# Optimization experiments

Hardware: AMD Instinct MI355X
Metric: run time of the kernel (lower is better)

## Reference

```python
import jax, jax.numpy as jnp
import numpy as np

B, T, V, C, L, H = 4, 1024, 32000, 768, 6, 12
HD = C // H  # head size 64
EPS = 1e-5


def _ln(x, s, b):
    mu = jnp.mean(x, axis=-1, keepdims=True)
    var = jnp.var(x, axis=-1, keepdims=True)
    return (x - mu) * jax.lax.rsqrt(var + EPS) * s + b


def setup_inputs() -> dict:
    key = jax.random.key(0)
    ks = jax.random.split(key, 12)
    p = lambda k, shape: jax.random.normal(k, shape, jnp.float32) * 0.02
    return {
        "idx": jax.random.randint(ks[0], (B, T), 0, V),
        "targets": jax.random.randint(ks[1], (B, T), 0, V),
        "tok_emb": p(ks[2], (V, C)),
        "pos_emb": p(ks[3], (T, C)),
        "Wq": p(ks[4], (L, H, C, HD)),
        "Wk": p(ks[5], (L, H, C, HD)),
        "Wv": p(ks[6], (L, H, C, HD)),
        "ln1_s": jnp.ones((L, C), jnp.float32),
        "ln1_b": jnp.zeros((L, C), jnp.float32),
        "ln2_s": jnp.ones((L, C), jnp.float32),
        "ln2_b": jnp.zeros((L, C), jnp.float32),
        "W1": p(ks[7], (L, C, 4 * C)),
        "b1": jnp.zeros((L, 4 * C), jnp.float32),
        "W2": p(ks[8], (L, 4 * C, C)),
        "b2": jnp.zeros((L, C), jnp.float32),
        "lnf_s": jnp.ones((C,), jnp.float32),
        "lnf_b": jnp.zeros((C,), jnp.float32),
        "Wout": p(ks[9], (C, V)),
        "bout": jnp.zeros((V,), jnp.float32),
    }


def reference(idx, targets, tok_emb, pos_emb, Wq, Wk, Wv, ln1_s, ln1_b, ln2_s, ln2_b,
              W1, b1, W2, b2, lnf_s, lnf_b, Wout, bout):
    x = tok_emb[idx] + pos_emb[None, :T, :]  # [B,T,C]
    mask = jnp.tril(jnp.ones((T, T), bool))
    scale = HD ** -0.5
    for l in range(L):  # fixed small layer count
        xn = _ln(x, ln1_s[l], ln1_b[l])
        q = jnp.einsum('btc,hcd->bhtd', xn, Wq[l])
        k = jnp.einsum('btc,hcd->bhtd', xn, Wk[l])
        v = jnp.einsum('btc,hcd->bhtd', xn, Wv[l])
        scores = jnp.einsum('bhtd,bhsd->bhts', q, k) * scale
        scores = jnp.where(mask[None, None], scores, -jnp.inf)
        w = jax.nn.softmax(scores, axis=-1)
        att = jnp.einsum('bhts,bhsd->bhtd', w, v)
        # concat heads in order, matching torch.cat over ModuleList
        x = x + att.transpose(0, 2, 1, 3).reshape(B, T, C)
        xn2 = _ln(x, ln2_s[l], ln2_b[l])
        h = jax.nn.relu(jnp.einsum('btc,cf->btf', xn2, W1[l]) + b1[l])
        x = x + jnp.einsum('btf,fc->btc', h, W2[l]) + b2[l]
    x = _ln(x, lnf_s, lnf_b)
    logits = jnp.einsum('btc,cv->btv', x, Wout) + bout
    logits = logits.reshape(B * T, V)
    lp = jax.nn.log_softmax(logits, axis=-1)
    loss = -jnp.mean(lp[jnp.arange(B * T), targets.reshape(-1)])
    return logits, loss
```

## Files before the change

kernel.cpp:

```cpp
#include <hip/hip_runtime.h>
#include <hip/hip_bf16.h>


typedef __attribute__((ext_vector_type(8))) short          bh8;
typedef __attribute__((ext_vector_type(4))) unsigned short us4;
typedef __attribute__((ext_vector_type(4))) float          fl4;

__device__ inline unsigned short f2b(float f) {
  unsigned u = __float_as_uint(f);
  return (unsigned short)((u + 0x7fffu + ((u >> 16) & 1u)) >> 16);
}

__global__ __launch_bounds__(256) void embed_kernel(
    const int* __restrict__ idx, const float* __restrict__ tok,
    const float* __restrict__ pos, float* __restrict__ x)
{
  int i = blockIdx.x * 256 + threadIdx.x;
  int bt = i / 768, c = i - bt * 768;
  int t = bt & 1023;
  x[i] = tok[(size_t)idx[bt] * 768 + c] + pos[t * 768 + c];
}

__global__ __launch_bounds__(256) void ln_bf16_kernel(
    const float* __restrict__ x, const float* __restrict__ s,
    const float* __restrict__ b, unsigned short* __restrict__ out)
{
  __shared__ float redS[4], redQ[4];
  int row = blockIdx.x, tid = threadIdx.x;
  const float* xr = x + (size_t)row * 768;
  float v0 = xr[tid], v1 = xr[tid + 256], v2 = xr[tid + 512];
  float sm = v0 + v1 + v2;
  float sq = v0 * v0 + v1 * v1 + v2 * v2;
#pragma unroll
  for (int m = 1; m < 64; m <<= 1) {
    sm += __shfl_xor(sm, m);
    sq += __shfl_xor(sq, m);
  }
  int wv = tid >> 6;
  if ((tid & 63) == 0) { redS[wv] = sm; redQ[wv] = sq; }
  __syncthreads();
  float ts = redS[0] + redS[1] + redS[2] + redS[3];
  float tq = redQ[0] + redQ[1] + redQ[2] + redQ[3];
  float mu = ts * (1.0f / 768.0f);
  float var = tq * (1.0f / 768.0f) - mu * mu;
  float inv = rsqrtf(var + 1e-5f);
  unsigned short* outr = out + (size_t)row * 768;
  outr[tid]       = f2b((v0 - mu) * inv * s[tid]       + b[tid]);
  outr[tid + 256] = f2b((v1 - mu) * inv * s[tid + 256] + b[tid + 256]);
  outr[tid + 512] = f2b((v2 - mu) * inv * s[tid + 512] + b[tid + 512]);
}

__global__ __launch_bounds__(256) void tconv_kernel(
    const float* __restrict__ src, unsigned short* __restrict__ dst,
    int K, int N)
{
  __shared__ float tt[64][65];
  int n0 = blockIdx.x * 64, k0 = blockIdx.y * 64;
  const float* s = src + (size_t)blockIdx.z * K * N;
  unsigned short* d = dst + (size_t)blockIdx.z * K * N;
  int tx = threadIdx.x & 63, g = threadIdx.x >> 6;
#pragma unroll
  for (int i = 0; i < 16; ++i) {
    int k = g * 16 + i;
    tt[k][tx] = s[(size_t)(k0 + k) * N + n0 + tx];
  }
  __syncthreads();
#pragma unroll
  for (int i = 0; i < 16; ++i) {
    int n = g * 16 + i;
    d[(size_t)(n0 + n) * K + k0 + tx] = f2b(tt[tx][n]);
  }
}

__global__ __launch_bounds__(256) void tqkv_kernel(
    const float* __restrict__ src, unsigned short* __restrict__ dst, int which)
{
  __shared__ float tt[64][65];
  int k0 = blockIdx.x * 64;
  int z = blockIdx.y;
  int l = z / 12, h = z - l * 12;
  const float* s = src + (size_t)z * 768 * 64;
  unsigned short* d = dst + (size_t)l * 2304 * 768 +
                      (size_t)(which * 768 + h * 64) * 768;
  int tx = threadIdx.x & 63, g = threadIdx.x >> 6;
#pragma unroll
  for (int i = 0; i < 16; ++i) {
    int k = g * 16 + i;
    tt[k][tx] = s[(size_t)(k0 + k) * 64 + tx];
  }
  __syncthreads();
#pragma unroll
  for (int i = 0; i < 16; ++i) {
    int n = g * 16 + i;
    d[(size_t)n * 768 + k0 + tx] = f2b(tt[tx][n]);
  }
}

template<int MODE>
__global__ __launch_bounds__(256) void gemm_bf16(
    const unsigned short* __restrict__ A, const unsigned short* __restrict__ Bt,
    const float* __restrict__ bias, float* __restrict__ OutF,
    unsigned short* __restrict__ OutH, int N, int K)
{
  __shared__ __align__(16) char As[128 * 64 * 2];
  __shared__ __align__(16) char Bs[128 * 64 * 2];
  const int tid = threadIdx.x;
  const int lane = tid & 63;
  const int wr = (tid >> 7) & 1, wc = (tid >> 6) & 1;
  const int m0 = blockIdx.y * 128, n0 = blockIdx.x * 128;
  const size_t Kb = (size_t)K * 2;

  fl4 acc[4][4] = {};
  const int o0 = tid * 16;
  const int rA = wr * 64 + (lane & 15);
  const int rB = wc * 64 + (lane & 15);
  const int kcol = (lane >> 4) << 4;
  const int sw = (lane & 7) << 4;

  auto ldAB = [&](int t, bh8* a, bh8* b) {
#pragma unroll
    for (int p = 0; p < 4; ++p) {
      int o = o0 + p * 4096;
      int row = o >> 7, col = o & 127;
      a[p] = *(const bh8*)((const char*)A + (size_t)(m0 + row) * Kb + (size_t)t * 128 + col);
      b[p] = *(const bh8*)((const char*)Bt + (size_t)(n0 + row) * Kb + (size_t)t * 128 + col);
    }
  };

  const int nK = K >> 6;
  bh8 ca[4], cb[4];
  ldAB(0, ca, cb);
  for (int t = 0; t < nK; ++t) {
    __syncthreads();
#pragma unroll
    for (int p = 0; p < 4; ++p) {
      int o = o0 + p * 4096;
      int row = o >> 7;
      int phys = o ^ ((row & 7) << 4);
      *(bh8*)(As + phys) = ca[p];
      *(bh8*)(Bs + phys) = cb[p];
    }
    __syncthreads();
    bh8 na[4], nb[4];
    const bool more = (t + 1 < nK);
    if (more) ldAB(t + 1, na, nb);
#pragma unroll
    for (int kh = 0; kh < 2; ++kh) {
      bh8 af[4], bf[4];
#pragma unroll
      for (int i = 0; i < 4; ++i) {
        af[i] = *(const bh8*)(As + (rA + i * 16) * 128 + ((kh * 64 + kcol) ^ sw));
        bf[i] = *(const bh8*)(Bs + (rB + i * 16) * 128 + ((kh * 64 + kcol) ^ sw));
      }
#pragma unroll
      for (int mi = 0; mi < 4; ++mi)
#pragma unroll
        for (int ni = 0; ni < 4; ++ni)
          acc[mi][ni] = __builtin_amdgcn_mfma_f32_16x16x32_bf16(
              af[mi], bf[ni], acc[mi][ni], 0, 0, 0);
    }
    if (more) {
#pragma unroll
      for (int p = 0; p < 4; ++p) { ca[p] = na[p]; cb[p] = nb[p]; }
    }
  }

  const int er = (lane >> 4) << 2;
  const int ec = lane & 15;
#pragma unroll
  for (int mi = 0; mi < 4; ++mi)
#pragma unroll
    for (int ni = 0; ni < 4; ++ni)
#pragma unroll
      for (int r = 0; r < 4; ++r) {
        int m = m0 + wr * 64 + mi * 16 + er + r;
        int n = n0 + wc * 64 + ni * 16 + ec;
        float v = acc[mi][ni][r];
        if (MODE == 0) {
          int which = n / 768, rem = n - which * 768;
          int hh = rem >> 6, dd = rem & 63;
          int bb = m >> 10, tt = m & 1023;
          size_t base = (size_t)(which * 48 + bb * 12 + hh) << 16;
          if (which == 2)
            OutH[base + (size_t)dd * 1024 + tt] = f2b(v);
          else
            OutH[base + (tt << 6) + dd] = f2b(v);
        } else if (MODE == 1) {
          v += bias[n]; v = fmaxf(v, 0.0f);
          OutH[(size_t)m * N + n] = f2b(v);
        } else {
          v += bias[n];
          OutF[(size_t)m * N + n] += v;
        }
      }
}

__global__ __launch_bounds__(256) void gemm_logits_bt(
    const unsigned short* __restrict__ A, const unsigned short* __restrict__ Bt,
    const float* __restrict__ bias, float* __restrict__ Out,
    float* __restrict__ pm, float* __restrict__ ps)
{
  __shared__ __align__(16) char As[128 * 64 * 2];
  __shared__ __align__(16) char Bs[128 * 64 * 2];
  const int tid = threadIdx.x;
  const int lane = tid & 63;
  const int wr = (tid >> 7) & 1, wc = (tid >> 6) & 1;
  const int bid = blockIdx.x;
  const int xcd = bid & 7, lb = bid >> 3;
  const int m_t = (xcd >> 1) * 8 + (lb & 7);
  const int n_t = (xcd & 1) * 125 + (lb >> 3);
  const int m0 = m_t * 128, n0 = n_t * 128;
  const size_t Kb = 1536;

  fl4 acc[4][4] = {};
  const int o0 = tid * 16;
  const int rA = wr * 64 + (lane & 15);
  const int rB = wc * 64 + (lane & 15);
  const int kcol = (lane >> 4) << 4;
  const int sw = (lane & 7) << 4;

  auto ldAB = [&](int t, bh8* a, bh8* b) {
#pragma unroll
    for (int p = 0; p < 4; ++p) {
      int o = o0 + p * 4096;
      int row = o >> 7, col = o & 127;
      a[p] = *(const bh8*)((const char*)A + (size_t)(m0 + row) * Kb + (size_t)t * 128 + col);
      b[p] = *(const bh8*)((const char*)Bt + (size_t)(n0 + row) * Kb + (size_t)t * 128 + col);
    }
  };

  const int nK = 12;
  bh8 ca[4], cb[4];
  ldAB(0, ca, cb);
  for (int t = 0; t < nK; ++t) {
    __syncthreads();
#pragma unroll
    for (int p = 0; p < 4; ++p) {
      int o = o0 + p * 4096;
      int row = o >> 7;
      int phys = o ^ ((row & 7) << 4);
      *(bh8*)(As + phys) = ca[p];
      *(bh8*)(Bs + phys) = cb[p];
    }
    __syncthreads();
    bh8 na[4], nb[4];
    const bool more = (t + 1 < nK);
    if (more) ldAB(t + 1, na, nb);
#pragma unroll
    for (int kh = 0; kh < 2; ++kh) {
      bh8 af[4], bf[4];
#pragma unroll
      for (int i = 0; i < 4; ++i) {
        af[i] = *(const bh8*)(As + (rA + i * 16) * 128 + ((kh * 64 + kcol) ^ sw));
        bf[i] = *(const bh8*)(Bs + (rB + i * 16) * 128 + ((kh * 64 + kcol) ^ sw));
      }
#pragma unroll
      for (int mi = 0; mi < 4; ++mi)
#pragma unroll
        for (int ni = 0; ni < 4; ++ni)
          acc[mi][ni] = __builtin_amdgcn_mfma_f32_16x16x32_bf16(
              af[mi], bf[ni], acc[mi][ni], 0, 0, 0);
    }
    if (more) {
#pragma unroll
      for (int p = 0; p < 4; ++p) { ca[p] = na[p]; cb[p] = nb[p]; }
    }
  }

  const int er = (lane >> 4) << 2;
  const int ec = lane & 15;
#pragma unroll
  for (int mi = 0; mi < 4; ++mi)
#pragma unroll
    for (int r = 0; r < 4; ++r) {
      int m = m0 + wr * 64 + mi * 16 + er + r;
      float tv[4];
#pragma unroll
      for (int ni = 0; ni < 4; ++ni) {
        int n = n0 + wc * 64 + ni * 16 + ec;
        tv[ni] = acc[mi][ni][r] + bias[n];
        __builtin_nontemporal_store(tv[ni], &Out[(size_t)m * 32000 + n]);
      }
      if (pm) {
        float mx = fmaxf(fmaxf(tv[0], tv[1]), fmaxf(tv[2], tv[3]));
#pragma unroll
        for (int msk = 1; msk < 16; msk <<= 1)
          mx = fmaxf(mx, __shfl_xor(mx, msk));
        float ss = __expf(tv[0] - mx) + __expf(tv[1] - mx) +
                   __expf(tv[2] - mx) + __expf(tv[3] - mx);
#pragma unroll
        for (int msk = 1; msk < 16; msk <<= 1)
          ss += __shfl_xor(ss, msk);
        if (ec == 0) {
          pm[(size_t)m * 500 + n_t * 2 + wc] = mx;
          ps[(size_t)m * 500 + n_t * 2 + wc] = ss;
        }
      }
    }
}

__global__ __launch_bounds__(256) void gemm_logits(
    const unsigned short* __restrict__ A, const float* __restrict__ W,
    const float* __restrict__ bias, float* __restrict__ Out)
{
  __shared__ __align__(16) char As[256 * 64 * 2];
  __shared__ __align__(16) char Bs[64 * 64 * 2];
  const int tid = threadIdx.x, lane = tid & 63, wid = tid >> 6;
  const int m0 = blockIdx.y * 256, n0 = blockIdx.x * 64;
  const size_t Kb = 1536;

  fl4 acc[4][4] = {};
  const int o0 = tid * 16;
  const int rA = wid * 64 + (lane & 15);
  const int rB = (lane & 15);
  const int kcol = (lane >> 4) << 4;
  const int sw = (lane & 7) << 4;
  const int bn = tid & 63, bg = tid >> 6;

  for (int t = 0; t < 12; ++t) {
    bh8 ra[8];
#pragma unroll
    for (int p = 0; p < 8; ++p) {
      int o = o0 + p * 4096;
      int row = o >> 7, col = o & 127;
      ra[p] = *(const bh8*)((const char*)A + (size_t)(m0 + row) * Kb + (size_t)t * 128 + col);
    }
    unsigned short rb[16];
#pragma unroll
    for (int p = 0; p < 4; ++p) {
      int q = p * 4 + bg;
#pragma unroll
      for (int i = 0; i < 4; ++i)
        rb[p * 4 + i] = f2b(W[(size_t)(t * 64 + q * 4 + i) * 32000 + n0 + bn]);
    }
    __syncthreads();
#pragma unroll
    for (int p = 0; p < 8; ++p) {
      int o = o0 + p * 4096;
      int row = o >> 7;
      *(bh8*)(As + (o ^ ((row & 7) << 4))) = ra[p];
    }
#pragma unroll
    for (int p = 0; p < 4; ++p) {
      int q = p * 4 + bg;
      int o = bn * 128 + q * 8;
      us4 w4 = { rb[p * 4], rb[p * 4 + 1], rb[p * 4 + 2], rb[p * 4 + 3] };
      *(us4*)(Bs + (o ^ ((bn & 7) << 4))) = w4;
    }
    __syncthreads();
#pragma unroll
    for (int kh = 0; kh < 2; ++kh) {
      bh8 af[4], bf[4];
#pragma unroll
      for (int i = 0; i < 4; ++i) {
        af[i] = *(const bh8*)(As + (rA + i * 16) * 128 + ((kh * 64 + kcol) ^ sw));
        bf[i] = *(const bh8*)(Bs + (rB + i * 16) * 128 + ((kh * 64 + kcol) ^ sw));
      }
#pragma unroll
      for (int mi = 0; mi < 4; ++mi)
#pragma unroll
        for (int ni = 0; ni < 4; ++ni)
          acc[mi][ni] = __builtin_amdgcn_mfma_f32_16x16x32_bf16(
              af[mi], bf[ni], acc[mi][ni], 0, 0, 0);
    }
    __syncthreads();
  }

  const int er = (lane >> 4) << 2, ec = lane & 15;
#pragma unroll
  for (int mi = 0; mi < 4; ++mi)
#pragma unroll
    for (int ni = 0; ni < 4; ++ni)
#pragma unroll
      for (int r = 0; r < 4; ++r) {
        int m = m0 + wid * 64 + mi * 16 + er + r;
        int n = n0 + ni * 16 + ec;
        __builtin_nontemporal_store(acc[mi][ni][r] + bias[n],
                                    &Out[(size_t)m * 32000 + n]);
      }
}

__global__ __launch_bounds__(128) void attn_mfma_kernel(
    const unsigned short* __restrict__ qkvb, float* __restrict__ x)
{
  __shared__ __align__(16) unsigned short Pls[2][32 * 72];
  __shared__ float MlLl[64];
  const int tid = threadIdx.x;
  const int lane = tid & 63, wv = tid >> 6;
  const int bh = blockIdx.y;
  const int b = bh / 12, h = bh - b * 12;
  const int qt = blockIdx.x, q0 = qt * 32;
  const int l15 = lane & 15, l4 = lane >> 4;
  const unsigned short* Qb = qkvb + ((size_t)bh << 16);
  const unsigned short* Kb = qkvb + ((size_t)(48 + bh) << 16);
  const unsigned short* Vb = qkvb + ((size_t)(96 + bh) << 16);
  unsigned short* Pl = Pls[wv];

  bh8 qf[2][2];
#pragma unroll
  for (int mi = 0; mi < 2; ++mi)
#pragma unroll
    for (int kh = 0; kh < 2; ++kh)
      qf[mi][kh] = *(const bh8*)(Qb + (size_t)(q0 + mi * 16 + l15) * 64 + kh * 32 + l4 * 8);

  fl4 o_acc[2][4] = {};
  fl4 m_run[2], l_run[2];
#pragma unroll
  for (int mi = 0; mi < 2; ++mi) {
    m_run[mi] = fl4{-3e38f, -3e38f, -3e38f, -3e38f};
    l_run[mi] = fl4{0.f, 0.f, 0.f, 0.f};
  }

  const int nkv = (qt >> 1) + 1;
  for (int j = wv; j < nkv; j += 2) {
    const int kv0 = j * 64;
    fl4 s[2][4] = {};
#pragma unroll
    for (int kh = 0; kh < 2; ++kh) {
      bh8 kf[4];
#pragma unroll
      for (int ni = 0; ni < 4; ++ni)
        kf[ni] = *(const bh8*)(Kb + (size_t)(kv0 + ni * 16 + l15) * 64 + kh * 32 + l4 * 8);
#pragma unroll
      for (int mi = 0; mi < 2; ++mi)
#pragma unroll
        for (int ni = 0; ni < 4; ++ni)
          s[mi][ni] = __builtin_amdgcn_mfma_f32_16x16x32_bf16(
              qf[mi][kh], kf[ni], s[mi][ni], 0, 0, 0);
    }

    const bool needmask = (kv0 + 63 > q0);
#pragma unroll
    for (int mi = 0; mi < 2; ++mi) {
#pragma unroll
      for (int r = 0; r < 4; ++r) {
        float mx = -3e38f;
#pragma unroll
        for (int ni = 0; ni < 4; ++ni) {
          float sv = s[mi][ni][r] * 0.125f;
          if (needmask) {
            int qg = q0 + mi * 16 + l4 * 4 + r;
            int kg = kv0 + ni * 16 + l15;
            if (kg > qg) sv = -3e38f;
          }
          s[mi][ni][r] = sv;
          mx = fmaxf(mx, sv);
        }
#pragma unroll
        for (int msk = 1; msk < 16; msk <<= 1)
          mx = fmaxf(mx, __shfl_xor(mx, msk));
        float mo = m_run[mi][r];
        float mn = fmaxf(mo, mx);
        float scale = __expf(mo - mn);
        float rsum = 0.f;
#pragma unroll
        for (int ni = 0; ni < 4; ++ni) {
          float p = __expf(s[mi][ni][r] - mn);
          s[mi][ni][r] = p;
          rsum += p;
        }
#pragma unroll
        for (int msk = 1; msk < 16; msk <<= 1)
          rsum += __shfl_xor(rsum, msk);
        m_run[mi][r] = mn;
        l_run[mi][r] = l_run[mi][r] * scale + rsum;
#pragma unroll
        for (int ni = 0; ni < 4; ++ni)
          o_acc[mi][ni][r] *= scale;
      }
#pragma unroll
      for (int ni = 0; ni < 4; ++ni)
#pragma unroll
        for (int r = 0; r < 4; ++r)
          Pl[(mi * 16 + l4 * 4 + r) * 72 + ni * 16 + l15] = f2b(s[mi][ni][r]);
    }

#pragma unroll
    for (int kh = 0; kh < 2; ++kh) {
      bh8 pf[2], vf[4];
#pragma unroll
      for (int mi = 0; mi < 2; ++mi)
        pf[mi] = *(const bh8*)(Pl + (mi * 16 + l15) * 72 + kh * 32 + l4 * 8);
#pragma unroll
      for (int ni = 0; ni < 4; ++ni)
        vf[ni] = *(const bh8*)(Vb + (size_t)(ni * 16 + l15) * 1024 + kv0 + kh * 32 + l4 * 8);
#pragma unroll
      for (int mi = 0; mi < 2; ++mi)
#pragma unroll
        for (int ni = 0; ni < 4; ++ni)
          o_acc[mi][ni] = __builtin_amdgcn_mfma_f32_16x16x32_bf16(
              pf[mi], vf[ni], o_acc[mi][ni], 0, 0, 0);
    }
  }

  __syncthreads();
  float* Ol = (float*)&Pls[0][0];
  if (wv == 1) {
#pragma unroll
    for (int mi = 0; mi < 2; ++mi)
#pragma unroll
      for (int r = 0; r < 4; ++r) {
        int row = mi * 16 + l4 * 4 + r;
        if (l15 == 0) { MlLl[row] = m_run[mi][r]; MlLl[32 + row] = l_run[mi][r]; }
#pragma unroll
        for (int ni = 0; ni < 4; ++ni)
          Ol[row * 68 + ni * 16 + l15] = o_acc[mi][ni][r];
      }
  }
  __syncthreads();
  if (wv == 0) {
#pragma unroll
    for (int mi = 0; mi < 2; ++mi)
#pragma unroll
      for (int r = 0; r < 4; ++r) {
        int row = mi * 16 + l4 * 4 + r;
        float m1 = MlLl[row], l1 = MlLl[32 + row];
        float m0v = m_run[mi][r];
        float mn = fmaxf(m0v, m1);
        float s0 = __expf(m0v - mn), s1 = __expf(m1 - mn);
        float inv = 1.0f / (l_run[mi][r] * s0 + l1 * s1);
        int q = q0 + row;
#pragma unroll
        for (int ni = 0; ni < 4; ++ni) {
          int d = ni * 16 + l15;
          float o = o_acc[mi][ni][r] * s0 + Ol[row * 68 + ni * 16 + l15] * s1;
          x[(size_t)(b * 1024 + q) * 768 + h * 64 + d] += o * inv;
        }
      }
  }
}

__global__ __launch_bounds__(256) void lossmerge_kernel(
    const float* __restrict__ pm, const float* __restrict__ ps,
    const float* __restrict__ logits, const int* __restrict__ targets,
    float* __restrict__ lrow)
{
  __shared__ float red[256];
  int row = blockIdx.x, tid = threadIdx.x;
  const float* pmr = pm + (size_t)row * 500;
  const float* psr = ps + (size_t)row * 500;
  float m = -3e38f;
  for (int i = tid; i < 500; i += 256) m = fmaxf(m, pmr[i]);
  red[tid] = m; __syncthreads();
  for (int o = 128; o > 0; o >>= 1) { if (tid < o) red[tid] = fmaxf(red[tid], red[tid + o]); __syncthreads(); }
  m = red[0]; __syncthreads();
  float s = 0.f;
  for (int i = tid; i < 500; i += 256) s += psr[i] * __expf(pmr[i] - m);
  red[tid] = s; __syncthreads();
  for (int o = 128; o > 0; o >>= 1) { if (tid < o) red[tid] += red[tid + o]; __syncthreads(); }
  if (tid == 0) {
    float lse = m + logf(red[0]);
    lrow[row] = (lse - logits[(size_t)row * 32000 + targets[row]]) * (1.0f / 4096.0f);
  }
}

__global__ __launch_bounds__(256) void lossrow_kernel(
    const float* __restrict__ logits, const int* __restrict__ targets,
    float* __restrict__ lrow)
{
  __shared__ float red[256];
  int row = blockIdx.x, tid = threadIdx.x;
  const float* lr = logits + (size_t)row * 32000;
  const float4* lr4 = (const float4*)lr;
  float lmax = -1e30f;
  for (int i = tid; i < 8000; i += 256) {
    float4 v = lr4[i];
    lmax = fmaxf(fmaxf(lmax, fmaxf(v.x, v.y)), fmaxf(v.z, v.w));
  }
  red[tid] = lmax; __syncthreads();
  for (int o = 128; o > 0; o >>= 1) { if (tid < o) red[tid] = fmaxf(red[tid], red[tid + o]); __syncthreads(); }
  float m = red[0]; __syncthreads();
  float ls = 0.f;
  for (int i = tid; i < 8000; i += 256) {
    float4 v = lr4[i];
    ls += expf(v.x - m) + expf(v.y - m) + expf(v.z - m) + expf(v.w - m);
  }
  red[tid] = ls; __syncthreads();
  for (int o = 128; o > 0; o >>= 1) { if (tid < o) red[tid] += red[tid + o]; __syncthreads(); }
  if (tid == 0) {
    float lse = m + logf(red[0]);
    lrow[row] = (lse - lr[targets[row]]) * (1.0f / 4096.0f);
  }
}

__global__ __launch_bounds__(256) void lossred_kernel(
    const float* __restrict__ lrow, float* __restrict__ out)
{
  __shared__ float red[256];
  int tid = threadIdx.x;
  float s = 0.f;
  for (int i = tid; i < 4096; i += 256) s += lrow[i];
  red[tid] = s; __syncthreads();
  for (int o = 128; o > 0; o >>= 1) { if (tid < o) red[tid] += red[tid + o]; __syncthreads(); }
  if (tid == 0) out[0] = red[0];
}

extern "C" void kernel_launch(void* const* d_in, const int* in_sizes, int n_in,
                              void* d_out, int out_size, void* d_ws, size_t ws_size,
                              hipStream_t stream)
{
  (void)in_sizes; (void)n_in; (void)out_size;
  const int Bq = 4, T = 1024, V = 32000, C = 768, L = 6;
  const int M = Bq * T;

  const int*   idx     = (const int*)d_in[0];
  const int*   targets = (const int*)d_in[1];
  const float* tok     = (const float*)d_in[2];
  const float* pos     = (const float*)d_in[3];
  const float* Wq      = (const float*)d_in[4];
  const float* Wk      = (const float*)d_in[5];
  const float* Wv      = (const float*)d_in[6];
  const float* ln1s    = (const float*)d_in[7];
  const float* ln1b    = (const float*)d_in[8];
  const float* ln2s    = (const float*)d_in[9];
  const float* ln2b    = (const float*)d_in[10];
  const float* W1      = (const float*)d_in[11];
  const float* b1      = (const float*)d_in[12];
  const float* W2      = (const float*)d_in[13];
  const float* b2      = (const float*)d_in[14];
  const float* lnfs    = (const float*)d_in[15];
  const float* lnfb    = (const float*)d_in[16];
  const float* Wout    = (const float*)d_in[17];
  const float* bout    = (const float*)d_in[18];
  float* out = (float*)d_out;

  char* ob = (char*)d_out;
  size_t oo = 0;
  auto oa = [&](size_t bytes) {
    void* p = ob + oo; oo += (bytes + 255) & ~(size_t)255; return p;
  };
  float*          x     = (float*)oa((size_t)M * C * 4);
  unsigned short* qkvb  = (unsigned short*)oa((size_t)3 * 48 * 65536 * 2);
  unsigned short* hb    = (unsigned short*)oa((size_t)M * 3072 * 2);
  unsigned short* Wqkvt = (unsigned short*)oa((size_t)L * 2304 * C * 2);
  unsigned short* W1t   = (unsigned short*)oa((size_t)L * C * 3072 * 2);
  unsigned short* W2t   = (unsigned short*)oa((size_t)L * C * 3072 * 2);

  char* wp = (char*)d_ws;
  unsigned short* xnb  = (unsigned short*)wp;
  float*          lrow = (float*)(wp + (size_t)M * C * 2);
  float*          pm   = (float*)(wp + (size_t)M * C * 2 + 16384);
  float*          ps   = pm + (size_t)M * 500;
  const size_t off_wbt_full  = (size_t)M * C * 2 + 16384 + (size_t)M * 500 * 8;
  const size_t off_wbt_small = (size_t)M * C * 2 + 16384;
  const size_t wbt_bytes = (size_t)V * C * 2;
  const bool full_ws = ws_size >= off_wbt_full + wbt_bytes;
  const bool wbt_ok  = full_ws || ws_size >= off_wbt_small + wbt_bytes;
  unsigned short* Wbt = (unsigned short*)(wp + (full_ws ? off_wbt_full
                                                        : off_wbt_small));

  embed_kernel<<<(M * C) / 256, 256, 0, stream>>>(idx, tok, pos, x);
  tqkv_kernel<<<dim3(12, 72), 256, 0, stream>>>(Wq, Wqkvt, 0);
  tqkv_kernel<<<dim3(12, 72), 256, 0, stream>>>(Wk, Wqkvt, 1);
  tqkv_kernel<<<dim3(12, 72), 256, 0, stream>>>(Wv, Wqkvt, 2);
  tconv_kernel<<<dim3(48, 12, 6), 256, 0, stream>>>(W1, W1t, C, 3072);
  tconv_kernel<<<dim3(12, 48, 6), 256, 0, stream>>>(W2, W2t, 3072, C);
  if (wbt_ok)
    tconv_kernel<<<dim3(500, 12, 1), 256, 0, stream>>>(Wout, Wbt, C, V);

  for (int l = 0; l < L; ++l) {
    ln_bf16_kernel<<<M, 256, 0, stream>>>(x, ln1s + l * C, ln1b + l * C, xnb);
    gemm_bf16<0><<<dim3(18, 32), 256, 0, stream>>>(
        xnb, Wqkvt + (size_t)l * 2304 * C, nullptr, nullptr, qkvb, 2304, C);
    attn_mfma_kernel<<<dim3(32, 48), 128, 0, stream>>>(qkvb, x);
    ln_bf16_kernel<<<M, 256, 0, stream>>>(x, ln2s + l * C, ln2b + l * C, xnb);
    gemm_bf16<1><<<dim3(24, 32), 256, 0, stream>>>(
        xnb, W1t + (size_t)l * C * 3072, b1 + (size_t)l * 3072, nullptr, hb, 3072, C);
    gemm_bf16<2><<<dim3(6, 32), 256, 0, stream>>>(
        hb, W2t + (size_t)l * C * 3072, b2 + (size_t)l * C, x, nullptr, C, 3072);
  }

  ln_bf16_kernel<<<M, 256, 0, stream>>>(x, lnfs, lnfb, xnb);
  if (wbt_ok)
    gemm_logits_bt<<<dim3(8000, 1), 256, 0, stream>>>(
        xnb, Wbt, bout, out, full_ws ? pm : nullptr, full_ws ? ps : nullptr);
  else
    gemm_logits<<<dim3(500, 16), 256, 0, stream>>>(xnb, Wout, bout, out);

  if (full_ws && wbt_ok)
    lossmerge_kernel<<<M, 256, 0, stream>>>(pm, ps, out, targets, lrow);
  else
    lossrow_kernel<<<M, 256, 0, stream>>>(out, targets, lrow);
  lossred_kernel<<<1, 256, 0, stream>>>(lrow, out + (size_t)M * V);
}
```

Before: 1.523 ms.

## Load logits GEMM fragments directly from global memory, bypassing LDS

Removes the LDS staging, swizzle and double-barrier loop from the logits GEMM. Each wave now loads its MFMA operand fragments straight from global memory, relying on L1/L2 to serve the reuse across waves. This drops the barriers and LDS traffic, but each block now fetches every A and B tile twice (once per wave pair) with 16-byte strided loads and no explicit prefetch overlap.

```diff
diff --git a/kernel.cpp b/kernel.cpp
--- a/kernel.cpp
+++ b/kernel.cpp
@@ -200,8 +200,6 @@
     const float* __restrict__ bias, float* __restrict__ Out,
     float* __restrict__ pm, float* __restrict__ ps)
 {
-  __shared__ __align__(16) char As[128 * 64 * 2];
-  __shared__ __align__(16) char Bs[128 * 64 * 2];
   const int tid = threadIdx.x;
   const int lane = tid & 63;
   const int wr = (tid >> 7) & 1, wc = (tid >> 6) & 1;
@@ -210,61 +208,33 @@
   const int m_t = (xcd >> 1) * 8 + (lb & 7);
   const int n_t = (xcd & 1) * 125 + (lb >> 3);
   const int m0 = m_t * 128, n0 = n_t * 128;
-  const size_t Kb = 1536;
 
   fl4 acc[4][4] = {};
-  const int o0 = tid * 16;
-  const int rA = wr * 64 + (lane & 15);
-  const int rB = wc * 64 + (lane & 15);
-  const int kcol = (lane >> 4) << 4;
-  const int sw = (lane & 7) << 4;
-
-  auto ldAB = [&](int t, bh8* a, bh8* b) {
-#pragma unroll
-    for (int p = 0; p < 4; ++p) {
-      int o = o0 + p * 4096;
-      int row = o >> 7, col = o & 127;
-      a[p] = *(const bh8*)((const char*)A + (size_t)(m0 + row) * Kb + (size_t)t * 128 + col);
-      b[p] = *(const bh8*)((const char*)Bt + (size_t)(n0 + row) * Kb + (size_t)t * 128 + col);
-    }
-  };
-
-  const int nK = 12;
-  bh8 ca[4], cb[4];
-  ldAB(0, ca, cb);
-  for (int t = 0; t < nK; ++t) {
-    __syncthreads();
-#pragma unroll
-    for (int p = 0; p < 4; ++p) {
-      int o = o0 + p * 4096;
-      int row = o >> 7;
-      int phys = o ^ ((row & 7) << 4);
-      *(bh8*)(As + phys) = ca[p];
-      *(bh8*)(Bs + phys) = cb[p];
-    }
-    __syncthreads();
-    bh8 na[4], nb[4];
-    const bool more = (t + 1 < nK);
-    if (more) ldAB(t + 1, na, nb);
-#pragma unroll
-    for (int kh = 0; kh < 2; ++kh) {
-      bh8 af[4], bf[4];
-#pragma unroll
-      for (int i = 0; i < 4; ++i) {
-        af[i] = *(const bh8*)(As + (rA + i * 16) * 128 + ((kh * 64 + kcol) ^ sw));
-        bf[i] = *(const bh8*)(Bs + (rB + i * 16) * 128 + ((kh * 64 + kcol) ^ sw));
-      }
-#pragma unroll
-      for (int mi = 0; mi < 4; ++mi)
-#pragma unroll
-        for (int ni = 0; ni < 4; ++ni)
-          acc[mi][ni] = __builtin_amdgcn_mfma_f32_16x16x32_bf16(
-              af[mi], bf[ni], acc[mi][ni], 0, 0, 0);
-    }
-    if (more) {
-#pragma unroll
-      for (int p = 0; p < 4; ++p) { ca[p] = na[p]; cb[p] = nb[p]; }
-    }
+  const int rrow = lane & 15;
+  const int kofs = (lane >> 4) * 8;
+
+  const unsigned short* Ar[4];
+  const unsigned short* Br[4];
+#pragma unroll
+  for (int i = 0; i < 4; ++i) {
+    Ar[i] = A  + (size_t)(m0 + wr * 64 + rrow + i * 16) * 768 + kofs;
+    Br[i] = Bt + (size_t)(n0 + wc * 64 + rrow + i * 16) * 768 + kofs;
+  }
+
+#pragma unroll 4
+  for (int ks = 0; ks < 24; ++ks) {
+    bh8 af[4], bf[4];
+#pragma unroll
+    for (int i = 0; i < 4; ++i) {
+      af[i] = *(const bh8*)(Ar[i] + ks * 32);
+      bf[i] = *(const bh8*)(Br[i] + ks * 32);
+    }
+#pragma unroll
+    for (int mi = 0; mi < 4; ++mi)
+#pragma unroll
+      for (int ni = 0; ni < 4; ++ni)
+        acc[mi][ni] = __builtin_amdgcn_mfma_f32_16x16x32_bf16(
+            af[mi], bf[ni], acc[mi][ni], 0, 0, 0);
   }
 
   const int er = (lane >> 4) << 2;
```

Measured after the change: 1.942 ms. 27.6% more time.

## Split-K the FFN down-projection and fuse partial sums into next LayerNorm

Applied to the files above, without the earlier changes.

The W2 GEMM (K=3072, only 192 blocks) is split into two K-halves across blockIdx.z, each writing a separate fp32 partial buffer. The following LayerNorm kernel (next layer's ln1 or the final LN) now adds both partials plus the bias into the residual x before normalizing. The aim is more blocks for the small-N GEMM to fill the GPU, and removal of the read-modify-write epilogue. The cost is an extra 2*M*C fp32 buffer carved from the output region and extra reads in the LN kernel.

```diff
diff --git a/kernel.cpp b/kernel.cpp
--- a/kernel.cpp
+++ b/kernel.cpp
@@ -50,6 +50,42 @@
   outr[tid + 512] = f2b((v2 - mu) * inv * s[tid + 512] + b[tid + 512]);
 }
 
+__global__ __launch_bounds__(256) void lnadd_bf16_kernel(
+    float* __restrict__ x, const float* __restrict__ P,
+    const float* __restrict__ Q, const float* __restrict__ badd,
+    const float* __restrict__ s, const float* __restrict__ b,
+    unsigned short* __restrict__ out)
+{
+  __shared__ float redS[4], redQ[4];
+  int row = blockIdx.x, tid = threadIdx.x;
+  float* xr = x + (size_t)row * 768;
+  const float* Pr = P + (size_t)row * 768;
+  const float* Qr = Q + (size_t)row * 768;
+  float v0 = xr[tid]       + Pr[tid]       + Qr[tid]       + badd[tid];
+  float v1 = xr[tid + 256] + Pr[tid + 256] + Qr[tid + 256] + badd[tid + 256];
+  float v2 = xr[tid + 512] + Pr[tid + 512] + Qr[tid + 512] + badd[tid + 512];
+  xr[tid] = v0; xr[tid + 256] = v1; xr[tid + 512] = v2;
+  float sm = v0 + v1 + v2;
+  float sq = v0 * v0 + v1 * v1 + v2 * v2;
+#pragma unroll
+  for (int m = 1; m < 64; m <<= 1) {
+    sm += __shfl_xor(sm, m);
+    sq += __shfl_xor(sq, m);
+  }
+  int wv = tid >> 6;
+  if ((tid & 63) == 0) { redS[wv] = sm; redQ[wv] = sq; }
+  __syncthreads();
+  float ts = redS[0] + redS[1] + redS[2] + redS[3];
+  float tq = redQ[0] + redQ[1] + redQ[2] + redQ[3];
+  float mu = ts * (1.0f / 768.0f);
+  float var = tq * (1.0f / 768.0f) - mu * mu;
+  float inv = rsqrtf(var + 1e-5f);
+  unsigned short* outr = out + (size_t)row * 768;
+  outr[tid]       = f2b((v0 - mu) * inv * s[tid]       + b[tid]);
+  outr[tid + 256] = f2b((v1 - mu) * inv * s[tid + 256] + b[tid + 256]);
+  outr[tid + 512] = f2b((v2 - mu) * inv * s[tid + 512] + b[tid + 512]);
+}
+
 __global__ __launch_bounds__(256) void tconv_kernel(
     const float* __restrict__ src, unsigned short* __restrict__ dst,
     int K, int N)
@@ -100,7 +136,7 @@
 __global__ __launch_bounds__(256) void gemm_bf16(
     const unsigned short* __restrict__ A, const unsigned short* __restrict__ Bt,
     const float* __restrict__ bias, float* __restrict__ OutF,
-    unsigned short* __restrict__ OutH, int N, int K)
+    unsigned short* __restrict__ OutH, int N, int K, int ld)
 {
   __shared__ __align__(16) char As[128 * 64 * 2];
   __shared__ __align__(16) char Bs[128 * 64 * 2];
@@ -108,7 +144,14 @@
   const int lane = tid & 63;
   const int wr = (tid >> 7) & 1, wc = (tid >> 6) & 1;
   const int m0 = blockIdx.y * 128, n0 = blockIdx.x * 128;
-  const size_t Kb = (size_t)K * 2;
+  const size_t Kb = (size_t)ld * 2;
+
+  if constexpr (MODE == 3) {
+    const int kz = blockIdx.z;
+    A    += (size_t)kz * 1536;
+    Bt   += (size_t)kz * 1536;
+    OutF += (size_t)kz * 4096 * 768;
+  }
 
   fl4 acc[4][4] = {};
   const int o0 = tid * 16;
@@ -188,9 +231,11 @@
         } else if (MODE == 1) {
           v += bias[n]; v = fmaxf(v, 0.0f);
           OutH[(size_t)m * N + n] = f2b(v);
-        } else {
+        } else if (MODE == 2) {
           v += bias[n];
           OutF[(size_t)m * N + n] += v;
+        } else {
+          OutF[(size_t)m * N + n] = v;
         }
       }
 }
@@ -635,6 +680,7 @@
   unsigned short* Wqkvt = (unsigned short*)oa((size_t)L * 2304 * C * 2);
   unsigned short* W1t   = (unsigned short*)oa((size_t)L * C * 3072 * 2);
   unsigned short* W2t   = (unsigned short*)oa((size_t)L * C * 3072 * 2);
+  float*          PQ    = (float*)oa((size_t)2 * M * C * 4);
 
   char* wp = (char*)d_ws;
   unsigned short* xnb  = (unsigned short*)wp;
@@ -659,18 +705,25 @@
     tconv_kernel<<<dim3(500, 12, 1), 256, 0, stream>>>(Wout, Wbt, C, V);
 
   for (int l = 0; l < L; ++l) {
-    ln_bf16_kernel<<<M, 256, 0, stream>>>(x, ln1s + l * C, ln1b + l * C, xnb);
+    if (l == 0)
+      ln_bf16_kernel<<<M, 256, 0, stream>>>(x, ln1s, ln1b, xnb);
+    else
+      lnadd_bf16_kernel<<<M, 256, 0, stream>>>(
+          x, PQ, PQ + (size_t)M * C, b2 + (size_t)(l - 1) * C,
+          ln1s + l * C, ln1b + l * C, xnb);
     gemm_bf16<0><<<dim3(18, 32), 256, 0, stream>>>(
-        xnb, Wqkvt + (size_t)l * 2304 * C, nullptr, nullptr, qkvb, 2304, C);
+        xnb, Wqkvt + (size_t)l * 2304 * C, nullptr, nullptr, qkvb, 2304, C, C);
     attn_mfma_kernel<<<dim3(32, 48), 128, 0, stream>>>(qkvb, x);
     ln_bf16_kernel<<<M, 256, 0, stream>>>(x, ln2s + l * C, ln2b + l * C, xnb);
     gemm_bf16<1><<<dim3(24, 32), 256, 0, stream>>>(
-        xnb, W1t + (size_t)l * C * 3072, b1 + (size_t)l * 3072, nullptr, hb, 3072, C);
-    gemm_bf16<2><<<dim3(6, 32), 256, 0, stream>>>(
-        hb, W2t + (size_t)l * C * 3072, b2 + (size_t)l * C, x, nullptr, C, 3072);
-  }
-
-  ln_bf16_kernel<<<M, 256, 0, stream>>>(x, lnfs, lnfb, xnb);
+        xnb, W1t + (size_t)l * C * 3072, b1 + (size_t)l * 3072, nullptr, hb,
+        3072, C, C);
+    gemm_bf16<3><<<dim3(6, 32, 2), 256, 0, stream>>>(
+        hb, W2t + (size_t)l * C * 3072, nullptr, PQ, nullptr, C, 1536, 3072);
+  }
+
+  lnadd_bf16_kernel<<<M, 256, 0, stream>>>(
+      x, PQ, PQ + (size_t)M * C, b2 + (size_t)(L - 1) * C, lnfs, lnfb, xnb);
   if (wbt_ok)
     gemm_logits_bt<<<dim3(8000, 1), 256, 0, stream>>>(
         xnb, Wbt, bout, out, full_ws ? pm : nullptr, full_ws ? ps : nullptr);
```

New measurement: 1.403 ms, median of 2. 1.08x faster.
